# Kernel tuning notes

Hardware: AMD Instinct MI355X
Metric: run time of the kernel (lower is better)

## Reference

```python
import jax, jax.numpy as jnp
import numpy as np

N_HEADS = 32
KV_HEADS = 8
HEAD_DIM = 64
THETA = 10000.0


def _rope_tables(L, head_dim, dtype):
    freqs = 1.0 / (THETA ** (jnp.arange(0, head_dim, 2, dtype=jnp.float32) / head_dim))
    phases = jnp.outer(jnp.arange(L, dtype=jnp.float32), freqs)  # [L, head_dim//2]
    phases = jnp.concatenate([phases, phases], axis=-1)          # [L, head_dim]
    return jnp.cos(phases).astype(dtype), jnp.sin(phases).astype(dtype)


def _rotate_half(x):
    x1, x2 = jnp.split(x, 2, axis=-1)
    return jnp.concatenate([-x2, x1], axis=-1)


def setup_inputs() -> dict:
    key = jax.random.key(0)
    ks = jax.random.split(key, 5)
    B, L, D = 2, 2048, 2048
    kv_dim = KV_HEADS * HEAD_DIM
    s = 0.02
    return {
        "x": jax.random.normal(ks[0], (B, L, D), jnp.float32),
        "wq": jax.random.normal(ks[1], (D, D), jnp.float32) * s,
        "wk": jax.random.normal(ks[2], (kv_dim, D), jnp.float32) * s,
        "wv": jax.random.normal(ks[3], (kv_dim, D), jnp.float32) * s,
        "wo": jax.random.normal(ks[4], (D, D), jnp.float32) * s,
    }


def reference(x, wq, wk, wv, wo):
    B, L, D = x.shape
    rep = N_HEADS // KV_HEADS
    cos, sin = _rope_tables(L, HEAD_DIM, x.dtype)  # [L, hd]

    # projections (torch Linear: y = x @ W.T)
    q = jnp.einsum('bld,ed->ble', x, wq).reshape(B, L, N_HEADS, HEAD_DIM).transpose(0, 2, 1, 3)   # [B,H,L,hd]
    k = jnp.einsum('bld,ed->ble', x, wk).reshape(B, L, KV_HEADS, HEAD_DIM).transpose(0, 2, 1, 3)  # [B,Hk,L,hd]
    v = jnp.einsum('bld,ed->ble', x, wv).reshape(B, L, KV_HEADS, HEAD_DIM).transpose(0, 2, 1, 3)

    # RoPE (broadcast over batch/heads)
    q = cos * q + _rotate_half(q) * sin
    k = cos * k + _rotate_half(k) * sin

    # GQA attention without materializing repeated K/V: group query heads per kv head
    qg = q.reshape(B, KV_HEADS, rep, L, HEAD_DIM)
    scale = 1.0 / jnp.sqrt(jnp.asarray(HEAD_DIM, x.dtype))
    scores = jnp.einsum('bkrqd,bkld->bkrql', qg, k) * scale  # [B,Hk,rep,L,L]
    causal = jnp.tril(jnp.ones((L, L), bool))
    scores = jnp.where(causal, scores, jnp.asarray(-jnp.inf, scores.dtype))
    attn = jax.nn.softmax(scores, axis=-1)
    out = jnp.einsum('bkrql,bkld->bkrqd', attn, v)           # [B,Hk,rep,L,hd]
    out = out.reshape(B, N_HEADS, L, HEAD_DIM).transpose(0, 2, 1, 3).reshape(B, L, D)
    return jnp.einsum('ble,de->bld', out, wo)
```

## Files before the change

### kernel.cpp

```cpp
#include <hip/hip_runtime.h>

typedef __attribute__((ext_vector_type(8))) __bf16 bf16x8;
typedef __attribute__((ext_vector_type(8))) ushort u16x8;
typedef __attribute__((ext_vector_type(4))) float f32x4;
typedef __attribute__((ext_vector_type(16))) float f32x16;

#define MFMA16(a, b, c) __builtin_amdgcn_mfma_f32_16x16x32_bf16(a, b, c, 0, 0, 0)
#define MFMA32(a, b, c) __builtin_amdgcn_mfma_f32_32x32x16_bf16(a, b, c, 0, 0, 0)

__device__ __forceinline__ ushort f2bf(float f) {
    union { float f; unsigned u; } v; v.f = f;
    unsigned r = v.u + 0x7FFFu + ((v.u >> 16) & 1u);
    return (ushort)(r >> 16);
}
__device__ __forceinline__ float bf2f(ushort b) {
    union { unsigned u; float f; } v; v.u = ((unsigned)b) << 16; return v.f;
}
__device__ __forceinline__ int cvtpk(float lo, float hi) {
    int r; asm("v_cvt_pk_bf16_f32 %0, %1, %2" : "=v"(r) : "v"(lo), "v"(hi)); return r;
}
__device__ __forceinline__ float fexp2(float x) {
    float r; asm("v_exp_f32 %0, %1" : "=v"(r) : "v"(x)); return r;
}
__device__ __forceinline__ void gload_lds16(const void* g, void* l) {
    __builtin_amdgcn_global_load_lds((const __attribute__((address_space(1))) void*)g,
                                     (__attribute__((address_space(3))) void*)l, 16, 0, 0);
}

__device__ __forceinline__ int swz8(int row, int g) {
    return row * 64 + (((g) ^ (row & 7)) << 3);
}
__device__ __forceinline__ int swz16(int row, int g) {
    return row * 128 + (((g) ^ (row & 15)) << 3);
}

__device__ __forceinline__ void stage64(const ushort* __restrict__ g, int rs,
                                        char* lds, int tid) {
    const int r = tid >> 3;
    const int c8 = ((tid & 7) ^ (r & 7)) << 3;
    const int wid = tid >> 6;
    gload_lds16(g + (size_t)r * rs + c8, lds + wid * 1024);
    gload_lds16(g + (size_t)(r + 32) * rs + c8, lds + 4096 + wid * 1024);
}

__device__ __forceinline__ void stageV128(const ushort* __restrict__ g, char* lds, int tid) {
    const int w = tid >> 6, l = tid & 63;
    const int g16 = l & 15;
#pragma unroll
    for (int j = 0; j < 4; ++j) {
        const int r = w * 16 + j * 4 + (l >> 4);
        gload_lds16(g + (size_t)r * 2048 + ((g16 ^ (r & 15)) << 3), lds + w * 4096 + j * 1024);
    }
}

__global__ void cvt_all(const float* __restrict__ x,  const float* __restrict__ wq,
                        const float* __restrict__ wk, const float* __restrict__ wv,
                        const float* __restrict__ wo, ushort* __restrict__ xb,
                        ushort* __restrict__ wcat, ushort* __restrict__ wob,
                        float* __restrict__ cosT, float* __restrict__ sinT) {
    int i = blockIdx.x * 256 + threadIdx.x;
    if (i >= 4718592) {
        int id = i - 4718592;
        if (id < 65536) {
            int fi = id >> 11, l = id & 2047;
            float freq = __expf(-(float)fi * (9.210340371976184f / 32.0f));
            float ph = (float)l * freq;
            cosT[id] = cosf(ph);
            sinT[id] = sinf(ph);
        }
        return;
    }
    const float* src; ushort* dst; int off;
    if (i < 2097152)      { src = x;  dst = xb;             off = i; }
    else if (i < 3145728) { src = wq; dst = wcat;           off = i - 2097152; }
    else if (i < 3407872) { src = wk; dst = wcat + 4194304; off = i - 3145728; }
    else if (i < 3670016) { src = wv; dst = wcat + 5242880; off = i - 3407872; }
    else                  { src = wo; dst = wob;            off = i - 3670016; }
    float4 v = ((const float4*)src)[off];
    ushort4 o;
    o.x = f2bf(v.x); o.y = f2bf(v.y); o.z = f2bf(v.z); o.w = f2bf(v.w);
    ((ushort4*)dst)[off] = o;
}

__global__ __launch_bounds__(512, 2) void gemmQKV64(const ushort* __restrict__ A,
                                                    const ushort* __restrict__ B,
                                                    ushort* __restrict__ qkv,
                                                    ushort* __restrict__ vt,
                                                    const float* __restrict__ cosT,
                                                    const float* __restrict__ sinT,
                                                    int K, int gx) {
    extern __shared__ __align__(16) ushort sm[];
    ushort* sA = sm;
    ushort* sB = sm + 32768;
    const int tid = threadIdx.x, lane = tid & 63, wid = tid >> 6;
    const int wr = wid >> 2, wc = wid & 3;
    const int lr = lane & 15, lg = lane >> 4;
    const int nwg = gridDim.x, bid = blockIdx.x;
    const int swz = (bid & 7) * (nwg >> 3) + (bid >> 3);
    const int m0 = (swz / gx) * 256, n0 = (swz % gx) * 256;
    const int NT = K >> 6;
    const int sr = tid >> 3;
    const int sc8 = ((tid & 7) ^ (sr & 7)) << 3;
    const ushort* gAt = A + (size_t)(m0 + sr) * K + sc8;
    const ushort* gBt = B + (size_t)(n0 + sr) * K + sc8;

    auto stgA = [&](int t, int buf) {
        const ushort* g = gAt + t * 64;
        char* ld = (char*)(sA + buf * 16384) + wid * 1024;
#pragma unroll
        for (int s = 0; s < 4; ++s)
            gload_lds16(g + (size_t)(s * 64) * K, ld + s * 8192);
    };
    auto stgB = [&](int t, int buf) {
        const ushort* g = gBt + t * 64;
        char* ld = (char*)(sB + buf * 16384) + wid * 1024;
#pragma unroll
        for (int s = 0; s < 4; ++s)
            gload_lds16(g + (size_t)(s * 64) * K, ld + s * 8192);
    };

    f32x4 acc[8][4] = {};
    stgA(0, 0); stgB(0, 0);
    stgA(1, 1); stgB(1, 1);
    asm volatile("s_waitcnt vmcnt(8)" ::: "memory");
    __builtin_amdgcn_s_barrier();

    for (int t = 0; t < NT; ++t) {
        const int c = t & 1;
        const ushort* Ac = sA + c * 16384 + (wr * 128) * 64;
        const ushort* Bc = sB + c * 16384 + (wc * 64) * 64;
        bf16x8 bfr[4][2];
#pragma unroll
        for (int nf = 0; nf < 4; ++nf)
#pragma unroll
            for (int kk = 0; kk < 2; ++kk)
                bfr[nf][kk] = *(const bf16x8*)&Bc[swz8(nf * 16 + lr, kk * 4 + lg)];
        bf16x8 af[4][2];
#pragma unroll
        for (int mf = 0; mf < 4; ++mf)
#pragma unroll
            for (int kk = 0; kk < 2; ++kk)
                af[mf][kk] = *(const bf16x8*)&Ac[swz8(mf * 16 + lr, kk * 4 + lg)];
        __builtin_amdgcn_s_setprio(1);
#pragma unroll
        for (int mf = 0; mf < 4; ++mf)
#pragma unroll
            for (int nf = 0; nf < 4; ++nf)
#pragma unroll
                for (int kk = 0; kk < 2; ++kk)
                    acc[mf][nf] = MFMA16(af[mf][kk], bfr[nf][kk], acc[mf][nf]);
        __builtin_amdgcn_s_setprio(0);
        bf16x8 af2[4][2];
#pragma unroll
        for (int mf = 0; mf < 4; ++mf)
#pragma unroll
            for (int kk = 0; kk < 2; ++kk)
                af2[mf][kk] = *(const bf16x8*)&Ac[swz8((mf + 4) * 16 + lr, kk * 4 + lg)];
        __builtin_amdgcn_s_setprio(1);
#pragma unroll
        for (int mf = 0; mf < 4; ++mf)
#pragma unroll
            for (int nf = 0; nf < 4; ++nf)
#pragma unroll
                for (int kk = 0; kk < 2; ++kk)
                    acc[mf + 4][nf] = MFMA16(af2[mf][kk], bfr[nf][kk], acc[mf + 4][nf]);
        __builtin_amdgcn_s_setprio(0);
        __builtin_amdgcn_s_barrier();
        if (t + 2 < NT) {
            stgA(t + 2, c); stgB(t + 2, c);
            asm volatile("s_waitcnt vmcnt(8)" ::: "memory");
        } else {
            asm volatile("s_waitcnt vmcnt(0)" ::: "memory");
        }
        __builtin_amdgcn_s_barrier();
    }

    const int r0 = m0 + wr * 128 + lg * 4;
    const int c0 = n0 + wc * 64 + lr;
    const int wavecol = n0 + wc * 64;
    if (wavecol >= 2560) {
        const int kh = (wavecol - 2560) >> 6;
        const int b = m0 >> 11;
        const int l0 = r0 & 2047;
#pragma unroll
        for (int ni = 0; ni < 4; ++ni) {
            const int d = lr + ni * 16;
            ushort* vrow = vt + (size_t)((b * 8 + kh) * 64 + d) * 2048 + l0;
#pragma unroll
            for (int mi = 0; mi < 8; ++mi) {
                ushort4 o;
                o.x = f2bf(acc[mi][ni][0]); o.y = f2bf(acc[mi][ni][1]);
                o.z = f2bf(acc[mi][ni][2]); o.w = f2bf(acc[mi][ni][3]);
                *(ushort4*)(vrow + mi * 16) = o;
            }
        }
    } else {
        const float scale = (wavecol < 2048) ? 0.18033688f : 1.0f;
        const int l0 = r0 & 2047;
#pragma unroll
        for (int ni = 0; ni < 2; ++ni) {
            const int i = ni * 16 + lr;
            const float* cp = cosT + i * 2048 + l0;
            const float* sp = sinT + i * 2048 + l0;
#pragma unroll
            for (int mi = 0; mi < 8; ++mi) {
                float4 cv = *(const float4*)(cp + mi * 16);
                float4 sv = *(const float4*)(sp + mi * 16);
#pragma unroll
                for (int r = 0; r < 4; ++r) {
                    float lo = acc[mi][ni][r], hi = acc[mi][ni + 2][r];
                    float c = ((const float*)&cv)[r], s = ((const float*)&sv)[r];
                    size_t row = (size_t)(r0 + mi * 16 + r) * 3072;
                    qkv[row + c0 + ni * 16]      = f2bf((c * lo - s * hi) * scale);
                    qkv[row + c0 + ni * 16 + 32] = f2bf((c * hi + s * lo) * scale);
                }
            }
        }
    }
}

__global__ __launch_bounds__(512, 2) void gemm64(const ushort* __restrict__ A,
                                                 const ushort* __restrict__ B,
                                                 float* __restrict__ C,
                                                 int M, int N, int K, int gx) {
    extern __shared__ __align__(16) ushort sm[];
    ushort* sA = sm;
    ushort* sB = sm + 32768;
    const int tid = threadIdx.x, lane = tid & 63, wid = tid >> 6;
    const int wr = wid >> 1, wc = wid & 1;
    const int lr = lane & 15, lg = lane >> 4;
    const int nwg = gridDim.x, bid = blockIdx.x;
    const int swz = (bid & 7) * (nwg >> 3) + (bid >> 3);
    const int m0 = (swz / gx) * 256, n0 = (swz % gx) * 128;
    const int NT = K >> 6;
    const int sr = tid >> 3;
    const int sc8 = ((tid & 7) ^ (sr & 7)) << 3;
    const ushort* gAt = A + (size_t)(m0 + sr) * K + sc8;
    const ushort* gBt = B + (size_t)(n0 + sr) * K + sc8;

    auto stgA = [&](int t, int buf) {
        const ushort* g = gAt + t * 64;
        char* ld = (char*)(sA + buf * 16384) + wid * 1024;
#pragma unroll
        for (int s = 0; s < 4; ++s)
            gload_lds16(g + (size_t)(s * 64) * K, ld + s * 8192);
    };
    auto stgB = [&](int t, int buf) {
        const ushort* g = gBt + t * 64;
        char* ld = (char*)(sB + buf * 8192) + wid * 1024;
        gload_lds16(g, ld);
        gload_lds16(g + (size_t)64 * K, ld + 8192);
    };

    f32x4 acc[4][4] = {};
    stgA(0, 0); stgB(0, 0);
    stgA(1, 1); stgB(1, 1);
    asm volatile("s_waitcnt vmcnt(6)" ::: "memory");
    __builtin_amdgcn_s_barrier();

    for (int t = 0; t < NT; ++t) {
        const int c = t & 1;
        const ushort* Ac = sA + c * 16384 + (wr * 64) * 64;
        const ushort* Bc = sB + c * 8192 + (wc * 64) * 64;
        bf16x8 af[4][2], bfr[4][2];
#pragma unroll
        for (int mf = 0; mf < 4; ++mf)
#pragma unroll
            for (int kk = 0; kk < 2; ++kk)
                af[mf][kk] = *(const bf16x8*)&Ac[swz8(mf * 16 + lr, kk * 4 + lg)];
#pragma unroll
        for (int nf = 0; nf < 4; ++nf)
#pragma unroll
            for (int kk = 0; kk < 2; ++kk)
                bfr[nf][kk] = *(const bf16x8*)&Bc[swz8(nf * 16 + lr, kk * 4 + lg)];
        __builtin_amdgcn_s_setprio(1);
#pragma unroll
        for (int mf = 0; mf < 4; ++mf)
#pragma unroll
            for (int nf = 0; nf < 4; ++nf)
#pragma unroll
                for (int kk = 0; kk < 2; ++kk)
                    acc[mf][nf] = MFMA16(af[mf][kk], bfr[nf][kk], acc[mf][nf]);
        __builtin_amdgcn_s_setprio(0);
        __builtin_amdgcn_s_barrier();
        if (t + 2 < NT) {
            stgA(t + 2, c); stgB(t + 2, c);
            asm volatile("s_waitcnt vmcnt(6)" ::: "memory");
        } else {
            asm volatile("s_waitcnt vmcnt(0)" ::: "memory");
        }
        __builtin_amdgcn_s_barrier();
    }

    const int r0 = m0 + wr * 64 + lg * 4;
    const int c0 = n0 + wc * 64 + lr;
#pragma unroll
    for (int mi = 0; mi < 4; ++mi)
#pragma unroll
        for (int ni = 0; ni < 4; ++ni)
#pragma unroll
            for (int r = 0; r < 4; ++r)
                C[(size_t)(r0 + mi * 16 + r) * N + c0 + ni * 16] = acc[mi][ni][r];
}

__global__ __launch_bounds__(256, 2) void attn_k(const ushort* __restrict__ qkv,
                                                 const ushort* __restrict__ vt,
                                                 ushort* __restrict__ attn) {
    extern __shared__ __align__(16) ushort smem[];
    const int tid = threadIdx.x, lane = tid & 63, wid = tid >> 6;
    const int hl = lane >> 5, lq = lane & 31;
    const int p = blockIdx.x;
    const int head = blockIdx.y, b = blockIdx.z;
    const int kh = head >> 2;

    const ushort* Kg = qkv + (size_t)(b * 2048) * 3072 + 2048 + kh * 64;
    const ushort* Vg = vt + (size_t)((b * 8 + kh) * 64) * 2048;

    for (int ph = 0; ph < 2; ++ph) {
        const int qt = ph ? p : 15 - p;
        const int qb = qt << 7;
        const int qw0 = qb + wid * 32;
        const int q_lane = qw0 + lq;
        const int nt = qt + 1;

        bf16x8 qf[4];
        {
            const ushort* qp = qkv + (size_t)(b * 2048 + qw0 + lq) * 3072 + head * 64 + hl * 8;
#pragma unroll
            for (int j = 0; j < 4; ++j) qf[j] = *(const bf16x8*)(qp + j * 16);
        }
        f32x16 o0 = {}, o1 = {};
        float lsum = 0.f;

        stage64(Kg, 3072, (char*)smem, tid);
        stage64(Kg + (size_t)64 * 3072, 3072, (char*)smem + 8192, tid);
        stageV128(Vg, (char*)(smem + 16384), tid);

        for (int it = 0; it < nt; ++it) {
            const int c = it & 1;
            const int kv0 = it << 7;
            const ushort* Kc = smem + c * 8192;
            const ushort* Vc = smem + 16384 + c * 8192;
            if (it + 1 < nt) {
                const int kv1 = kv0 + 128;
                char* kd = (char*)smem + (c ^ 1) * 16384;
                char* vd = (char*)(smem + 16384) + (c ^ 1) * 16384;
                stage64(Kg + (size_t)kv1 * 3072, 3072, kd, tid);
                stage64(Kg + (size_t)(kv1 + 64) * 3072, 3072, kd + 8192, tid);
                stageV128(Vg + kv1, vd, tid);
                asm volatile("s_waitcnt vmcnt(8)" ::: "memory");
            } else {
                asm volatile("s_waitcnt vmcnt(0)" ::: "memory");
            }
            __builtin_amdgcn_s_barrier();

            f32x16 s0 = {}, s1 = {}, s2 = {}, s3 = {};
            __builtin_amdgcn_s_setprio(1);
#pragma unroll
            for (int j = 0; j < 4; ++j) {
                bf16x8 k0 = *(const bf16x8*)&Kc[swz8(lq, j * 2 + hl)];
                bf16x8 k1 = *(const bf16x8*)&Kc[swz8(32 + lq, j * 2 + hl)];
                bf16x8 k2 = *(const bf16x8*)&Kc[swz8(64 + lq, j * 2 + hl)];
                bf16x8 k3 = *(const bf16x8*)&Kc[swz8(96 + lq, j * 2 + hl)];
                s0 = MFMA32(k0, qf[j], s0);
                s1 = MFMA32(k1, qf[j], s1);
                s2 = MFMA32(k2, qf[j], s2);
                s3 = MFMA32(k3, qf[j], s3);
            }
            __builtin_amdgcn_s_setprio(0);

            if (it == qt) {
#pragma unroll
                for (int i = 0; i < 16; ++i) {
                    int r = (i & 3) + ((i >> 2) << 3) + (hl << 2) + kv0;
                    if (r > q_lane)      s0[i] = -1e30f;
                    if (r + 32 > q_lane) s1[i] = -1e30f;
                    if (r + 64 > q_lane) s2[i] = -1e30f;
                    if (r + 96 > q_lane) s3[i] = -1e30f;
                }
            }
#pragma unroll
            for (int i = 0; i < 16; ++i) s0[i] = fexp2(s0[i]);
#pragma unroll
            for (int i = 0; i < 16; ++i) s1[i] = fexp2(s1[i]);
#pragma unroll
            for (int i = 0; i < 16; ++i) s2[i] = fexp2(s2[i]);
#pragma unroll
            for (int i = 0; i < 16; ++i) s3[i] = fexp2(s3[i]);
            f32x16 ts = (s0 + s1) + (s2 + s3);
            float u0 = ts[0] + ts[1], u1 = ts[2] + ts[3], u2 = ts[4] + ts[5], u3 = ts[6] + ts[7];
            float u4 = ts[8] + ts[9], u5 = ts[10] + ts[11], u6 = ts[12] + ts[13], u7 = ts[14] + ts[15];
            float rs = ((u0 + u1) + (u2 + u3)) + ((u4 + u5) + (u6 + u7));
            {
                auto sw = __builtin_amdgcn_permlane32_swap(__float_as_int(rs), __float_as_int(rs), 0, 0);
                rs = __int_as_float(sw[0]) + __int_as_float(sw[1]);
            }
            lsum += rs;

            bf16x8 pf[8];
#define PFB(cc, q0, q1, q2, q3, q4, q5, q6, q7)                                   \
            {                                                                      \
                int pk01 = cvtpk(q0, q1), pk23 = cvtpk(q2, q3);                    \
                int pk45 = cvtpk(q4, q5), pk67 = cvtpk(q6, q7);                    \
                auto sA = __builtin_amdgcn_permlane32_swap(pk01, pk45, 0, 0);      \
                auto sB = __builtin_amdgcn_permlane32_swap(pk23, pk67, 0, 0);      \
                union { int w[4]; bf16x8 v; } u;                                   \
                u.w[0] = sA[0]; u.w[1] = sB[0]; u.w[2] = sA[1]; u.w[3] = sB[1];    \
                pf[cc] = u.v;                                                      \
            }
            PFB(0, s0[0], s0[1], s0[2], s0[3], s0[4], s0[5], s0[6], s0[7])
            PFB(1, s0[8], s0[9], s0[10], s0[11], s0[12], s0[13], s0[14], s0[15])
            PFB(2, s1[0], s1[1], s1[2], s1[3], s1[4], s1[5], s1[6], s1[7])
            PFB(3, s1[8], s1[9], s1[10], s1[11], s1[12], s1[13], s1[14], s1[15])
            PFB(4, s2[0], s2[1], s2[2], s2[3], s2[4], s2[5], s2[6], s2[7])
            PFB(5, s2[8], s2[9], s2[10], s2[11], s2[12], s2[13], s2[14], s2[15])
            PFB(6, s3[0], s3[1], s3[2], s3[3], s3[4], s3[5], s3[6], s3[7])
            PFB(7, s3[8], s3[9], s3[10], s3[11], s3[12], s3[13], s3[14], s3[15])
#undef PFB
            __builtin_amdgcn_s_setprio(1);
#pragma unroll
            for (int cc = 0; cc < 8; ++cc) {
                bf16x8 v0 = *(const bf16x8*)&Vc[swz16(lq, cc * 2 + hl)];
                bf16x8 v1 = *(const bf16x8*)&Vc[swz16(32 + lq, cc * 2 + hl)];
                o0 = MFMA32(v0, pf[cc], o0);
                o1 = MFMA32(v1, pf[cc], o1);
            }
            __builtin_amdgcn_s_setprio(0);
            __builtin_amdgcn_s_barrier();
        }

        __syncthreads();
        ushort* sc = (ushort*)((char*)smem + wid * 4096);
        float inv = 1.0f / lsum;
#pragma unroll
        for (int i = 0; i < 16; i += 2) {
            int d0 = (i & 3) + ((i >> 2) << 3) + (hl << 2);
            int g0 = d0 >> 3, g1 = (d0 + 32) >> 3;
            *(int*)&sc[lq * 64 + ((g0 ^ (lq & 7)) << 3) + (d0 & 7)] = cvtpk(o0[i] * inv, o0[i + 1] * inv);
            *(int*)&sc[lq * 64 + ((g1 ^ (lq & 7)) << 3) + (d0 & 7)] = cvtpk(o1[i] * inv, o1[i + 1] * inv);
        }
        __syncthreads();
        {
            const int q = lane >> 1, db = (lane & 1) << 5;
            const size_t orow = (size_t)(b * 2048 + qb + wid * 32 + q);
#pragma unroll
            for (int j = 0; j < 4; ++j) {
                int g = (db >> 3) + j;
                u16x8 v = *(const u16x8*)&sc[q * 64 + ((g ^ (q & 7)) << 3)];
                *(u16x8*)(attn + orow * 2048 + head * 64 + g * 8) = v;
            }
        }
        __syncthreads();
    }
}

extern "C" void kernel_launch(void* const* d_in, const int* in_sizes, int n_in,
                              void* d_out, int out_size, void* d_ws, size_t ws_size,
                              hipStream_t stream) {
    const float* x  = (const float*)d_in[0];
    const float* wq = (const float*)d_in[1];
    const float* wk = (const float*)d_in[2];
    const float* wv = (const float*)d_in[3];
    const float* wo = (const float*)d_in[4];
    float* out = (float*)d_out;
    char* ws = (char*)d_ws;

    ushort* xb   = (ushort*)(ws);
    ushort* wcat = (ushort*)(ws + 16777216);
    ushort* wob  = (ushort*)(ws + 29360128);
    ushort* qkv  = (ushort*)(ws + 37748736);
    ushort* vt   = (ushort*)(ws + 62914560);
    ushort* attn = (ushort*)(ws + 67108864);
    float*  cosT = (float*)(ws + 83886080);
    float*  sinT = (float*)(ws + 84148224);

    (void)hipFuncSetAttribute((const void*)gemmQKV64,
                              hipFuncAttributeMaxDynamicSharedMemorySize, 131072);
    (void)hipFuncSetAttribute((const void*)gemm64,
                              hipFuncAttributeMaxDynamicSharedMemorySize, 98304);
    (void)hipFuncSetAttribute((const void*)attn_k,
                              hipFuncAttributeMaxDynamicSharedMemorySize, 65536);

    cvt_all<<<18688, 256, 0, stream>>>(x, wq, wk, wv, wo, xb, wcat, wob, cosT, sinT);
    gemmQKV64<<<192, 512, 131072, stream>>>(xb, wcat, qkv, vt, cosT, sinT, 2048, 12);
    attn_k<<<dim3(8, 32, 2), 256, 65536, stream>>>(qkv, vt, attn);
    gemm64<<<256, 512, 98304, stream>>>(attn, wob, out, 4096, 2048, 2048, 16);
}
```

Baseline: 175.5 us.

## Restructure QKV and output GEMM main loops into 8-wave fine-grained phased pipeline

Both GEMM kernels replace the double-buffered two-tile prefetch loop with a finer schedule. Each K-step is split into phases, and a slice of the next tile's global-to-LDS loads is issued in each phase, interleaved with barriers and a subset of MFMAs. The wave-to-tile mapping changes so that each wave reads A or B from a half-tile region. The goal is better overlap of memory loads with MFMA work. In exchange the loop has more barriers per iteration and prefetches only one tile ahead instead of two.

```diff
diff --git a/kernel.cpp b/kernel.cpp
--- a/kernel.cpp
+++ b/kernel.cpp
@@ -82,13 +82,13 @@
     ((ushort4*)dst)[off] = o;
 }
 
-__global__ __launch_bounds__(512, 2) void gemmQKV64(const ushort* __restrict__ A,
-                                                    const ushort* __restrict__ B,
-                                                    ushort* __restrict__ qkv,
-                                                    ushort* __restrict__ vt,
-                                                    const float* __restrict__ cosT,
-                                                    const float* __restrict__ sinT,
-                                                    int K, int gx) {
+__global__ __launch_bounds__(512, 2) void gemmQKV8(const ushort* __restrict__ A,
+                                                   const ushort* __restrict__ B,
+                                                   ushort* __restrict__ qkv,
+                                                   ushort* __restrict__ vt,
+                                                   const float* __restrict__ cosT,
+                                                   const float* __restrict__ sinT,
+                                                   int K, int gx) {
     extern __shared__ __align__(16) ushort sm[];
     ushort* sA = sm;
     ushort* sB = sm + 32768;
@@ -104,75 +104,61 @@
     const ushort* gAt = A + (size_t)(m0 + sr) * K + sc8;
     const ushort* gBt = B + (size_t)(n0 + sr) * K + sc8;
 
-    auto stgA = [&](int t, int buf) {
-        const ushort* g = gAt + t * 64;
-        char* ld = (char*)(sA + buf * 16384) + wid * 1024;
-#pragma unroll
-        for (int s = 0; s < 4; ++s)
-            gload_lds16(g + (size_t)(s * 64) * K, ld + s * 8192);
+    auto stageH = [&](int t, int h, int buf) {
+        const ushort* g = (h < 2 ? gAt + (size_t)(h * 128) * K
+                                 : gBt + (size_t)((h - 2) * 128) * K) + t * 64;
+        char* ld = (char*)((h < 2) ? (sA + buf * 16384 + h * 8192)
+                                   : (sB + buf * 16384 + (h - 2) * 8192)) + wid * 1024;
+        gload_lds16(g, ld);
+        gload_lds16(g + (size_t)64 * K, ld + 8192);
     };
-    auto stgB = [&](int t, int buf) {
-        const ushort* g = gBt + t * 64;
-        char* ld = (char*)(sB + buf * 16384) + wid * 1024;
-#pragma unroll
-        for (int s = 0; s < 4; ++s)
-            gload_lds16(g + (size_t)(s * 64) * K, ld + s * 8192);
-    };
 
     f32x4 acc[8][4] = {};
-    stgA(0, 0); stgB(0, 0);
-    stgA(1, 1); stgB(1, 1);
-    asm volatile("s_waitcnt vmcnt(8)" ::: "memory");
-    __builtin_amdgcn_s_barrier();
-
-    for (int t = 0; t < NT; ++t) {
-        const int c = t & 1;
-        const ushort* Ac = sA + c * 16384 + (wr * 128) * 64;
-        const ushort* Bc = sB + c * 16384 + (wc * 64) * 64;
-        bf16x8 bfr[4][2];
-#pragma unroll
-        for (int nf = 0; nf < 4; ++nf)
-#pragma unroll
-            for (int kk = 0; kk < 2; ++kk)
-                bfr[nf][kk] = *(const bf16x8*)&Bc[swz8(nf * 16 + lr, kk * 4 + lg)];
-        bf16x8 af[4][2];
-#pragma unroll
-        for (int mf = 0; mf < 4; ++mf)
-#pragma unroll
-            for (int kk = 0; kk < 2; ++kk)
-                af[mf][kk] = *(const bf16x8*)&Ac[swz8(mf * 16 + lr, kk * 4 + lg)];
-        __builtin_amdgcn_s_setprio(1);
-#pragma unroll
-        for (int mf = 0; mf < 4; ++mf)
-#pragma unroll
-            for (int nf = 0; nf < 4; ++nf)
-#pragma unroll
-                for (int kk = 0; kk < 2; ++kk)
-                    acc[mf][nf] = MFMA16(af[mf][kk], bfr[nf][kk], acc[mf][nf]);
-        __builtin_amdgcn_s_setprio(0);
-        bf16x8 af2[4][2];
-#pragma unroll
-        for (int mf = 0; mf < 4; ++mf)
-#pragma unroll
-            for (int kk = 0; kk < 2; ++kk)
-                af2[mf][kk] = *(const bf16x8*)&Ac[swz8((mf + 4) * 16 + lr, kk * 4 + lg)];
-        __builtin_amdgcn_s_setprio(1);
-#pragma unroll
-        for (int mf = 0; mf < 4; ++mf)
-#pragma unroll
-            for (int nf = 0; nf < 4; ++nf)
-#pragma unroll
-                for (int kk = 0; kk < 2; ++kk)
-                    acc[mf + 4][nf] = MFMA16(af2[mf][kk], bfr[nf][kk], acc[mf + 4][nf]);
-        __builtin_amdgcn_s_setprio(0);
-        __builtin_amdgcn_s_barrier();
-        if (t + 2 < NT) {
-            stgA(t + 2, c); stgB(t + 2, c);
-            asm volatile("s_waitcnt vmcnt(8)" ::: "memory");
-        } else {
-            asm volatile("s_waitcnt vmcnt(0)" ::: "memory");
-        }
-        __builtin_amdgcn_s_barrier();
+    stageH(0, 0, 0); stageH(0, 1, 0); stageH(0, 2, 0); stageH(0, 3, 0);
+
+    const int NI = NT >> 1;
+    for (int i = 0; i < NI; ++i) {
+#pragma unroll
+        for (int half = 0; half < 2; ++half) {
+            const int cur = half;
+            const int st = 2 * i + 1 + half;
+            const ushort* Ac = sA + cur * 16384 + wr * 8192;
+            const ushort* Bc = sB + cur * 16384 + (wc >> 1) * 8192;
+            const int brow = (wc & 1) * 64;
+            bf16x8 bfr[4][2];
+#pragma unroll
+            for (int p = 0; p < 4; ++p) {
+                if (st < NT) stageH(st, p, cur ^ 1);
+                if (p == 0) {
+                    if (st < NT) asm volatile("s_waitcnt vmcnt(2)" ::: "memory");
+                    else         asm volatile("s_waitcnt vmcnt(0)" ::: "memory");
+                }
+                __builtin_amdgcn_s_barrier();
+                if (p == 0) {
+#pragma unroll
+                    for (int nf = 0; nf < 4; ++nf)
+#pragma unroll
+                        for (int kk = 0; kk < 2; ++kk)
+                            bfr[nf][kk] = *(const bf16x8*)&Bc[swz8(brow + nf * 16 + lr, kk * 4 + lg)];
+                }
+                bf16x8 af[2][2];
+#pragma unroll
+                for (int mi = 0; mi < 2; ++mi)
+#pragma unroll
+                    for (int kk = 0; kk < 2; ++kk)
+                        af[mi][kk] = *(const bf16x8*)&Ac[swz8((p * 2 + mi) * 16 + lr, kk * 4 + lg)];
+                __builtin_amdgcn_s_setprio(1);
+#pragma unroll
+                for (int mi = 0; mi < 2; ++mi)
+#pragma unroll
+                    for (int nf = 0; nf < 4; ++nf)
+#pragma unroll
+                        for (int kk = 0; kk < 2; ++kk)
+                            acc[p * 2 + mi][nf] = MFMA16(af[mi][kk], bfr[nf][kk], acc[p * 2 + mi][nf]);
+                __builtin_amdgcn_s_setprio(0);
+                __builtin_amdgcn_s_barrier();
+            }
+        }
     }
 
     const int r0 = m0 + wr * 128 + lg * 4;
@@ -219,10 +205,10 @@
     }
 }
 
-__global__ __launch_bounds__(512, 2) void gemm64(const ushort* __restrict__ A,
+__global__ __launch_bounds__(512, 2) void gemmO8(const ushort* __restrict__ A,
                                                  const ushort* __restrict__ B,
                                                  float* __restrict__ C,
-                                                 int M, int N, int K, int gx) {
+                                                 int N, int K, int gx) {
     extern __shared__ __align__(16) ushort sm[];
     ushort* sA = sm;
     ushort* sB = sm + 32768;
@@ -238,58 +224,64 @@
     const ushort* gAt = A + (size_t)(m0 + sr) * K + sc8;
     const ushort* gBt = B + (size_t)(n0 + sr) * K + sc8;
 
-    auto stgA = [&](int t, int buf) {
-        const ushort* g = gAt + t * 64;
-        char* ld = (char*)(sA + buf * 16384) + wid * 1024;
-#pragma unroll
-        for (int s = 0; s < 4; ++s)
-            gload_lds16(g + (size_t)(s * 64) * K, ld + s * 8192);
-    };
-    auto stgB = [&](int t, int buf) {
-        const ushort* g = gBt + t * 64;
-        char* ld = (char*)(sB + buf * 8192) + wid * 1024;
+    auto stageH = [&](int t, int h, int buf) {
+        const ushort* g = (h < 2 ? gAt + (size_t)(h * 128) * K : gBt) + t * 64;
+        char* ld = (char*)((h < 2) ? (sA + buf * 16384 + h * 8192)
+                                   : (sB + buf * 8192)) + wid * 1024;
         gload_lds16(g, ld);
         gload_lds16(g + (size_t)64 * K, ld + 8192);
     };
 
     f32x4 acc[4][4] = {};
-    stgA(0, 0); stgB(0, 0);
-    stgA(1, 1); stgB(1, 1);
-    asm volatile("s_waitcnt vmcnt(6)" ::: "memory");
-    __builtin_amdgcn_s_barrier();
-
-    for (int t = 0; t < NT; ++t) {
-        const int c = t & 1;
-        const ushort* Ac = sA + c * 16384 + (wr * 64) * 64;
-        const ushort* Bc = sB + c * 8192 + (wc * 64) * 64;
-        bf16x8 af[4][2], bfr[4][2];
-#pragma unroll
-        for (int mf = 0; mf < 4; ++mf)
-#pragma unroll
-            for (int kk = 0; kk < 2; ++kk)
-                af[mf][kk] = *(const bf16x8*)&Ac[swz8(mf * 16 + lr, kk * 4 + lg)];
-#pragma unroll
-        for (int nf = 0; nf < 4; ++nf)
-#pragma unroll
-            for (int kk = 0; kk < 2; ++kk)
-                bfr[nf][kk] = *(const bf16x8*)&Bc[swz8(nf * 16 + lr, kk * 4 + lg)];
-        __builtin_amdgcn_s_setprio(1);
-#pragma unroll
-        for (int mf = 0; mf < 4; ++mf)
-#pragma unroll
-            for (int nf = 0; nf < 4; ++nf)
-#pragma unroll
-                for (int kk = 0; kk < 2; ++kk)
-                    acc[mf][nf] = MFMA16(af[mf][kk], bfr[nf][kk], acc[mf][nf]);
-        __builtin_amdgcn_s_setprio(0);
-        __builtin_amdgcn_s_barrier();
-        if (t + 2 < NT) {
-            stgA(t + 2, c); stgB(t + 2, c);
-            asm volatile("s_waitcnt vmcnt(6)" ::: "memory");
-        } else {
-            asm volatile("s_waitcnt vmcnt(0)" ::: "memory");
-        }
-        __builtin_amdgcn_s_barrier();
+    stageH(0, 0, 0); stageH(0, 1, 0); stageH(0, 2, 0);
+
+    const int NI = NT >> 1;
+    for (int i = 0; i < NI; ++i) {
+#pragma unroll
+        for (int half = 0; half < 2; ++half) {
+            const int cur = half;
+            const int st = 2 * i + 1 + half;
+            const ushort* Ac = sA + cur * 16384 + (wr >> 1) * 8192;
+            const int arow = (wr & 1) * 64;
+            const ushort* Bc = sB + cur * 8192;
+            const int brow = wc * 64;
+            bf16x8 bfr[4][2];
+#pragma unroll
+            for (int p = 0; p < 2; ++p) {
+                if (st < NT) {
+                    if (p == 0) { stageH(st, 0, cur ^ 1); stageH(st, 1, cur ^ 1); }
+                    else        { stageH(st, 2, cur ^ 1); }
+                }
+                if (p == 0) {
+                    if (st < NT) asm volatile("s_waitcnt vmcnt(4)" ::: "memory");
+                    else         asm volatile("s_waitcnt vmcnt(0)" ::: "memory");
+                }
+                __builtin_amdgcn_s_barrier();
+                if (p == 0) {
+#pragma unroll
+                    for (int nf = 0; nf < 4; ++nf)
+#pragma unroll
+                        for (int kk = 0; kk < 2; ++kk)
+                            bfr[nf][kk] = *(const bf16x8*)&Bc[swz8(brow + nf * 16 + lr, kk * 4 + lg)];
+                }
+                bf16x8 af[2][2];
+#pragma unroll
+                for (int mi = 0; mi < 2; ++mi)
+#pragma unroll
+                    for (int kk = 0; kk < 2; ++kk)
+                        af[mi][kk] = *(const bf16x8*)&Ac[swz8(arow + (p * 2 + mi) * 16 + lr, kk * 4 + lg)];
+                __builtin_amdgcn_s_setprio(1);
+#pragma unroll
+                for (int mi = 0; mi < 2; ++mi)
+#pragma unroll
+                    for (int nf = 0; nf < 4; ++nf)
+#pragma unroll
+                        for (int kk = 0; kk < 2; ++kk)
+                            acc[p * 2 + mi][nf] = MFMA16(af[mi][kk], bfr[nf][kk], acc[p * 2 + mi][nf]);
+                __builtin_amdgcn_s_setprio(0);
+                __builtin_amdgcn_s_barrier();
+            }
+        }
     }
 
     const int r0 = m0 + wr * 64 + lg * 4;
@@ -474,15 +466,15 @@
     float*  cosT = (float*)(ws + 83886080);
     float*  sinT = (float*)(ws + 84148224);
 
-    (void)hipFuncSetAttribute((const void*)gemmQKV64,
+    (void)hipFuncSetAttribute((const void*)gemmQKV8,
                               hipFuncAttributeMaxDynamicSharedMemorySize, 131072);
-    (void)hipFuncSetAttribute((const void*)gemm64,
+    (void)hipFuncSetAttribute((const void*)gemmO8,
                               hipFuncAttributeMaxDynamicSharedMemorySize, 98304);
     (void)hipFuncSetAttribute((const void*)attn_k,
                               hipFuncAttributeMaxDynamicSharedMemorySize, 65536);
 
     cvt_all<<<18688, 256, 0, stream>>>(x, wq, wk, wv, wo, xb, wcat, wob, cosT, sinT);
-    gemmQKV64<<<192, 512, 131072, stream>>>(xb, wcat, qkv, vt, cosT, sinT, 2048, 12);
+    gemmQKV8<<<192, 512, 131072, stream>>>(xb, wcat, qkv, vt, cosT, sinT, 2048, 12);
     attn_k<<<dim3(8, 32, 2), 256, 65536, stream>>>(qkv, vt, attn);
-    gemm64<<<256, 512, 98304, stream>>>(attn, wob, out, 4096, 2048, 2048, 16);
-}
+    gemmO8<<<256, 512, 98304, stream>>>(attn, wob, out, 2048, 2048, 16);
+}
```

New measurement: 166.9 us (median of 2 runs). 4.9% less time.

## Restructure QKV and output GEMMs into two-phase pipelined main loops

Applied to the files above, without the earlier changes.

Both GEMM kernels change from prefetching two tiles ahead to a one-ahead double buffer. Each K-step is split into two half-phases, and loads of the next B tile and the next A tile are interleaved with MFMA work on the current A halves, using explicit lgkmcnt waits and sched barriers. The output GEMM also remaps its waves to a 2x4 grid with 128x32 per-wave tiles to match that schedule. This aims to hide global-to-LDS latency and LDS read latency behind MFMA work, at the cost of a shallower prefetch and an extra barrier per iteration.

```diff
diff --git a/kernel.cpp b/kernel.cpp
--- a/kernel.cpp
+++ b/kernel.cpp
@@ -82,7 +82,7 @@
     ((ushort4*)dst)[off] = o;
 }
 
-__global__ __launch_bounds__(512, 2) void gemmQKV64(const ushort* __restrict__ A,
+__global__ __launch_bounds__(512, 2) void gemmQKV2p(const ushort* __restrict__ A,
                                                     const ushort* __restrict__ B,
                                                     ushort* __restrict__ qkv,
                                                     ushort* __restrict__ vt,
@@ -104,75 +104,90 @@
     const ushort* gAt = A + (size_t)(m0 + sr) * K + sc8;
     const ushort* gBt = B + (size_t)(n0 + sr) * K + sc8;
 
-    auto stgA = [&](int t, int buf) {
-        const ushort* g = gAt + t * 64;
-        char* ld = (char*)(sA + buf * 16384) + wid * 1024;
+    auto stgB = [&](int t, int buf) {
+        const ushort* g = gBt + t * 64;
+        char* ld = (char*)(sB + buf * 16384) + wid * 1024;
 #pragma unroll
         for (int s = 0; s < 4; ++s)
             gload_lds16(g + (size_t)(s * 64) * K, ld + s * 8192);
     };
-    auto stgB = [&](int t, int buf) {
-        const ushort* g = gBt + t * 64;
-        char* ld = (char*)(sB + buf * 16384) + wid * 1024;
-#pragma unroll
-        for (int s = 0; s < 4; ++s)
-            gload_lds16(g + (size_t)(s * 64) * K, ld + s * 8192);
+    auto stgA_L0 = [&](int t, int buf) {
+        const ushort* g = gAt + t * 64;
+        char* ld = (char*)(sA + buf * 16384) + wid * 1024;
+        gload_lds16(g, ld);
+        gload_lds16(g + (size_t)128 * K, ld + 2 * 8192);
     };
+    auto stgA_L1 = [&](int t, int buf) {
+        const ushort* g = gAt + t * 64;
+        char* ld = (char*)(sA + buf * 16384) + wid * 1024;
+        gload_lds16(g + (size_t)64 * K, ld + 8192);
+        gload_lds16(g + (size_t)192 * K, ld + 3 * 8192);
+    };
 
     f32x4 acc[8][4] = {};
-    stgA(0, 0); stgB(0, 0);
-    stgA(1, 1); stgB(1, 1);
-    asm volatile("s_waitcnt vmcnt(8)" ::: "memory");
+    stgB(0, 0); stgA_L0(0, 0); stgA_L1(0, 0);
+    asm volatile("s_waitcnt vmcnt(0)" ::: "memory");
     __builtin_amdgcn_s_barrier();
 
     for (int t = 0; t < NT; ++t) {
-        const int c = t & 1;
-        const ushort* Ac = sA + c * 16384 + (wr * 128) * 64;
-        const ushort* Bc = sB + c * 16384 + (wc * 64) * 64;
-        bf16x8 bfr[4][2];
+        const int cur = t & 1;
+        const ushort* Ac = sA + cur * 16384 + wr * 8192;
+        const ushort* Bc = sB + cur * 16384 + (wc >> 1) * 8192;
+        const int brow = (wc & 1) * 64;
+        bf16x8 bfr[4][2], a01[4][2];
 #pragma unroll
         for (int nf = 0; nf < 4; ++nf)
 #pragma unroll
             for (int kk = 0; kk < 2; ++kk)
-                bfr[nf][kk] = *(const bf16x8*)&Bc[swz8(nf * 16 + lr, kk * 4 + lg)];
-        bf16x8 af[4][2];
+                bfr[nf][kk] = *(const bf16x8*)&Bc[swz8(brow + nf * 16 + lr, kk * 4 + lg)];
 #pragma unroll
         for (int mf = 0; mf < 4; ++mf)
 #pragma unroll
             for (int kk = 0; kk < 2; ++kk)
-                af[mf][kk] = *(const bf16x8*)&Ac[swz8(mf * 16 + lr, kk * 4 + lg)];
-        __builtin_amdgcn_s_setprio(1);
-#pragma unroll
-        for (int mf = 0; mf < 4; ++mf)
-#pragma unroll
-            for (int nf = 0; nf < 4; ++nf)
-#pragma unroll
-                for (int kk = 0; kk < 2; ++kk)
-                    acc[mf][nf] = MFMA16(af[mf][kk], bfr[nf][kk], acc[mf][nf]);
-        __builtin_amdgcn_s_setprio(0);
-        bf16x8 af2[4][2];
-#pragma unroll
-        for (int mf = 0; mf < 4; ++mf)
-#pragma unroll
-            for (int kk = 0; kk < 2; ++kk)
-                af2[mf][kk] = *(const bf16x8*)&Ac[swz8((mf + 4) * 16 + lr, kk * 4 + lg)];
-        __builtin_amdgcn_s_setprio(1);
-#pragma unroll
-        for (int mf = 0; mf < 4; ++mf)
-#pragma unroll
-            for (int nf = 0; nf < 4; ++nf)
-#pragma unroll
-                for (int kk = 0; kk < 2; ++kk)
-                    acc[mf + 4][nf] = MFMA16(af2[mf][kk], bfr[nf][kk], acc[mf + 4][nf]);
-        __builtin_amdgcn_s_setprio(0);
-        __builtin_amdgcn_s_barrier();
-        if (t + 2 < NT) {
-            stgA(t + 2, c); stgB(t + 2, c);
-            asm volatile("s_waitcnt vmcnt(8)" ::: "memory");
+                a01[mf][kk] = *(const bf16x8*)&Ac[swz8(mf * 16 + lr, kk * 4 + lg)];
+        if (t + 1 < NT) {
+            stgB(t + 1, cur ^ 1);
+            asm volatile("s_waitcnt vmcnt(4)" ::: "memory");
         } else {
             asm volatile("s_waitcnt vmcnt(0)" ::: "memory");
         }
         __builtin_amdgcn_s_barrier();
+        asm volatile("s_waitcnt lgkmcnt(0)" ::: "memory");
+        __builtin_amdgcn_sched_barrier(0);
+        __builtin_amdgcn_s_setprio(1);
+#pragma unroll
+        for (int mf = 0; mf < 4; ++mf)
+#pragma unroll
+            for (int nf = 0; nf < 4; ++nf)
+#pragma unroll
+                for (int kk = 0; kk < 2; ++kk)
+                    acc[mf][nf] = MFMA16(a01[mf][kk], bfr[nf][kk], acc[mf][nf]);
+        __builtin_amdgcn_s_setprio(0);
+        bf16x8 a23[4][2];
+#pragma unroll
+        for (int mf = 0; mf < 4; ++mf)
+#pragma unroll
+            for (int kk = 0; kk < 2; ++kk)
+                a23[mf][kk] = *(const bf16x8*)&Ac[swz8(64 + mf * 16 + lr, kk * 4 + lg)];
+        if (t + 1 < NT) {
+            stgA_L0(t + 1, cur ^ 1);
+            stgA_L1(t + 1, cur ^ 1);
+            asm volatile("s_waitcnt vmcnt(2)" ::: "memory");
+        } else {
+            asm volatile("s_waitcnt vmcnt(0)" ::: "memory");
+        }
+        __builtin_amdgcn_s_barrier();
+        asm volatile("s_waitcnt lgkmcnt(0)" ::: "memory");
+        __builtin_amdgcn_sched_barrier(0);
+        __builtin_amdgcn_s_setprio(1);
+#pragma unroll
+        for (int mf = 0; mf < 4; ++mf)
+#pragma unroll
+            for (int nf = 0; nf < 4; ++nf)
+#pragma unroll
+                for (int kk = 0; kk < 2; ++kk)
+                    acc[mf + 4][nf] = MFMA16(a23[mf][kk], bfr[nf][kk], acc[mf + 4][nf]);
+        __builtin_amdgcn_s_setprio(0);
     }
 
     const int r0 = m0 + wr * 128 + lg * 4;
@@ -219,15 +234,15 @@
     }
 }
 
-__global__ __launch_bounds__(512, 2) void gemm64(const ushort* __restrict__ A,
-                                                 const ushort* __restrict__ B,
-                                                 float* __restrict__ C,
-                                                 int M, int N, int K, int gx) {
+__global__ __launch_bounds__(512, 2) void gemmO2p(const ushort* __restrict__ A,
+                                                  const ushort* __restrict__ B,
+                                                  float* __restrict__ C,
+                                                  int N, int K, int gx) {
     extern __shared__ __align__(16) ushort sm[];
     ushort* sA = sm;
     ushort* sB = sm + 32768;
     const int tid = threadIdx.x, lane = tid & 63, wid = tid >> 6;
-    const int wr = wid >> 1, wc = wid & 1;
+    const int wr = wid >> 2, wc = wid & 3;
     const int lr = lane & 15, lg = lane >> 4;
     const int nwg = gridDim.x, bid = blockIdx.x;
     const int swz = (bid & 7) * (nwg >> 3) + (bid >> 3);
@@ -238,66 +253,97 @@
     const ushort* gAt = A + (size_t)(m0 + sr) * K + sc8;
     const ushort* gBt = B + (size_t)(n0 + sr) * K + sc8;
 
-    auto stgA = [&](int t, int buf) {
-        const ushort* g = gAt + t * 64;
-        char* ld = (char*)(sA + buf * 16384) + wid * 1024;
-#pragma unroll
-        for (int s = 0; s < 4; ++s)
-            gload_lds16(g + (size_t)(s * 64) * K, ld + s * 8192);
-    };
     auto stgB = [&](int t, int buf) {
         const ushort* g = gBt + t * 64;
         char* ld = (char*)(sB + buf * 8192) + wid * 1024;
         gload_lds16(g, ld);
         gload_lds16(g + (size_t)64 * K, ld + 8192);
     };
-
-    f32x4 acc[4][4] = {};
-    stgA(0, 0); stgB(0, 0);
-    stgA(1, 1); stgB(1, 1);
-    asm volatile("s_waitcnt vmcnt(6)" ::: "memory");
+    auto stgA_L0 = [&](int t, int buf) {
+        const ushort* g = gAt + t * 64;
+        char* ld = (char*)(sA + buf * 16384) + wid * 1024;
+        gload_lds16(g, ld);
+        gload_lds16(g + (size_t)128 * K, ld + 2 * 8192);
+    };
+    auto stgA_L1 = [&](int t, int buf) {
+        const ushort* g = gAt + t * 64;
+        char* ld = (char*)(sA + buf * 16384) + wid * 1024;
+        gload_lds16(g + (size_t)64 * K, ld + 8192);
+        gload_lds16(g + (size_t)192 * K, ld + 3 * 8192);
+    };
+
+    f32x4 acc[8][2] = {};
+    stgB(0, 0); stgA_L0(0, 0); stgA_L1(0, 0);
+    asm volatile("s_waitcnt vmcnt(0)" ::: "memory");
     __builtin_amdgcn_s_barrier();
 
     for (int t = 0; t < NT; ++t) {
-        const int c = t & 1;
-        const ushort* Ac = sA + c * 16384 + (wr * 64) * 64;
-        const ushort* Bc = sB + c * 8192 + (wc * 64) * 64;
-        bf16x8 af[4][2], bfr[4][2];
-#pragma unroll
-        for (int mf = 0; mf < 4; ++mf)
+        const int cur = t & 1;
+        const ushort* Ac = sA + cur * 16384 + wr * 8192;
+        const ushort* Bc = sB + cur * 8192;
+        const int brow = wc * 32;
+        bf16x8 bfr[2][2], a01[4][2];
+#pragma unroll
+        for (int nf = 0; nf < 2; ++nf)
 #pragma unroll
             for (int kk = 0; kk < 2; ++kk)
-                af[mf][kk] = *(const bf16x8*)&Ac[swz8(mf * 16 + lr, kk * 4 + lg)];
-#pragma unroll
-        for (int nf = 0; nf < 4; ++nf)
+                bfr[nf][kk] = *(const bf16x8*)&Bc[swz8(brow + nf * 16 + lr, kk * 4 + lg)];
+#pragma unroll
+        for (int mf = 0; mf < 4; ++mf)
 #pragma unroll
             for (int kk = 0; kk < 2; ++kk)
-                bfr[nf][kk] = *(const bf16x8*)&Bc[swz8(nf * 16 + lr, kk * 4 + lg)];
-        __builtin_amdgcn_s_setprio(1);
-#pragma unroll
-        for (int mf = 0; mf < 4; ++mf)
-#pragma unroll
-            for (int nf = 0; nf < 4; ++nf)
-#pragma unroll
-                for (int kk = 0; kk < 2; ++kk)
-                    acc[mf][nf] = MFMA16(af[mf][kk], bfr[nf][kk], acc[mf][nf]);
-        __builtin_amdgcn_s_setprio(0);
-        __builtin_amdgcn_s_barrier();
-        if (t + 2 < NT) {
-            stgA(t + 2, c); stgB(t + 2, c);
-            asm volatile("s_waitcnt vmcnt(6)" ::: "memory");
+                a01[mf][kk] = *(const bf16x8*)&Ac[swz8(mf * 16 + lr, kk * 4 + lg)];
+        if (t + 1 < NT) {
+            stgB(t + 1, cur ^ 1);
+            asm volatile("s_waitcnt vmcnt(2)" ::: "memory");
         } else {
             asm volatile("s_waitcnt vmcnt(0)" ::: "memory");
         }
         __builtin_amdgcn_s_barrier();
+        asm volatile("s_waitcnt lgkmcnt(0)" ::: "memory");
+        __builtin_amdgcn_sched_barrier(0);
+        __builtin_amdgcn_s_setprio(1);
+#pragma unroll
+        for (int mf = 0; mf < 4; ++mf)
+#pragma unroll
+            for (int nf = 0; nf < 2; ++nf)
+#pragma unroll
+                for (int kk = 0; kk < 2; ++kk)
+                    acc[mf][nf] = MFMA16(a01[mf][kk], bfr[nf][kk], acc[mf][nf]);
+        __builtin_amdgcn_s_setprio(0);
+        bf16x8 a23[4][2];
+#pragma unroll
+        for (int mf = 0; mf < 4; ++mf)
+#pragma unroll
+            for (int kk = 0; kk < 2; ++kk)
+                a23[mf][kk] = *(const bf16x8*)&Ac[swz8(64 + mf * 16 + lr, kk * 4 + lg)];
+        if (t + 1 < NT) {
+            stgA_L0(t + 1, cur ^ 1);
+            stgA_L1(t + 1, cur ^ 1);
+            asm volatile("s_waitcnt vmcnt(2)" ::: "memory");
+        } else {
+            asm volatile("s_waitcnt vmcnt(0)" ::: "memory");
+        }
+        __builtin_amdgcn_s_barrier();
+        asm volatile("s_waitcnt lgkmcnt(0)" ::: "memory");
+        __builtin_amdgcn_sched_barrier(0);
+        __builtin_amdgcn_s_setprio(1);
+#pragma unroll
+        for (int mf = 0; mf < 4; ++mf)
+#pragma unroll
+            for (int nf = 0; nf < 2; ++nf)
+#pragma unroll
+                for (int kk = 0; kk < 2; ++kk)
+                    acc[mf + 4][nf] = MFMA16(a23[mf][kk], bfr[nf][kk], acc[mf + 4][nf]);
+        __builtin_amdgcn_s_setprio(0);
     }
 
-    const int r0 = m0 + wr * 64 + lg * 4;
-    const int c0 = n0 + wc * 64 + lr;
-#pragma unroll
-    for (int mi = 0; mi < 4; ++mi)
-#pragma unroll
-        for (int ni = 0; ni < 4; ++ni)
+    const int r0 = m0 + wr * 128 + lg * 4;
+    const int c0 = n0 + wc * 32 + lr;
+#pragma unroll
+    for (int mi = 0; mi < 8; ++mi)
+#pragma unroll
+        for (int ni = 0; ni < 2; ++ni)
 #pragma unroll
             for (int r = 0; r < 4; ++r)
                 C[(size_t)(r0 + mi * 16 + r) * N + c0 + ni * 16] = acc[mi][ni][r];
@@ -474,15 +520,15 @@
     float*  cosT = (float*)(ws + 83886080);
     float*  sinT = (float*)(ws + 84148224);
 
-    (void)hipFuncSetAttribute((const void*)gemmQKV64,
+    (void)hipFuncSetAttribute((const void*)gemmQKV2p,
                               hipFuncAttributeMaxDynamicSharedMemorySize, 131072);
-    (void)hipFuncSetAttribute((const void*)gemm64,
+    (void)hipFuncSetAttribute((const void*)gemmO2p,
                               hipFuncAttributeMaxDynamicSharedMemorySize, 98304);
     (void)hipFuncSetAttribute((const void*)attn_k,
                               hipFuncAttributeMaxDynamicSharedMemorySize, 65536);
 
     cvt_all<<<18688, 256, 0, stream>>>(x, wq, wk, wv, wo, xb, wcat, wob, cosT, sinT);
-    gemmQKV64<<<192, 512, 131072, stream>>>(xb, wcat, qkv, vt, cosT, sinT, 2048, 12);
+    gemmQKV2p<<<192, 512, 131072, stream>>>(xb, wcat, qkv, vt, cosT, sinT, 2048, 12);
     attn_k<<<dim3(8, 32, 2), 256, 65536, stream>>>(qkv, vt, attn);
-    gemm64<<<256, 512, 98304, stream>>>(attn, wob, out, 4096, 2048, 2048, 16);
-}
+    gemmO2p<<<256, 512, 98304, stream>>>(attn, wob, out, 2048, 2048, 16);
+}
```

New measurement: 176.6 us. Within noise of the previous version (+0.6%).
